# Performance work log

Measured on AMD Instinct MI355X. Metric: run time of the kernel, lower is better.

The kernel has to match this reference:

```python
import jax, jax.numpy as jnp
from jax import lax
import numpy as np

ROI = 7  # roi_size


def _extract_rois(feat, coords):
    """Faithful port of extract_roi_features: clamp a 7x7 window to image bounds,
    then bilinearly resize the (possibly smaller) crop back to 7x7
    (F.interpolate, mode='bilinear', align_corners=False)."""
    B, C, H, W = feat.shape
    half = ROI // 2

    def axis_idx(c, size):
        start = jnp.maximum(0, c - half)                  # [B,A]
        end = jnp.minimum(size, c + half + 1)
        Li = end - start                                  # crop length (int) [B,A]
        L = Li.astype(feat.dtype)[..., None]              # [B,A,1]
        j = jnp.arange(ROI, dtype=feat.dtype)
        # align_corners=False source coordinate, clamped into the crop
        src = jnp.clip((j + 0.5) * L / ROI - 0.5, 0.0, L - 1.0)  # [B,A,7]
        i0 = jnp.floor(src).astype(jnp.int32)
        i1 = jnp.minimum(i0 + 1, Li[..., None] - 1)
        w1 = src - i0.astype(feat.dtype)
        return start[..., None] + i0, start[..., None] + i1, 1.0 - w1, w1

    xc = coords[..., 0].astype(jnp.int32)
    yc = coords[..., 1].astype(jnp.int32)
    y0, y1, wy0, wy1 = axis_idx(yc, H)
    x0, x1, wx0, wx1 = axis_idx(xc, W)
    Bn, A = xc.shape
    bi = jnp.arange(Bn)[:, None, None, None]

    def g(Y, X):  # gather -> [B,A,7,7,C]
        return feat[bi, :, Y[:, :, :, None], X[:, :, None, :]]

    wy0 = wy0[:, :, :, None, None]; wy1 = wy1[:, :, :, None, None]
    wx0 = wx0[:, :, None, :, None]; wx1 = wx1[:, :, None, :, None]
    v = (wy0 * wx0 * g(y0, x0) + wy0 * wx1 * g(y0, x1)
         + wy1 * wx0 * g(y1, x0) + wy1 * wx1 * g(y1, x1))
    return jnp.transpose(v, (0, 1, 4, 2, 3))  # [B,A,C,7,7]


def _conv(x, w, b, pad):
    y = lax.conv_general_dilated(x, w, (1, 1), [(pad, pad), (pad, pad)],
                                 dimension_numbers=('NCHW', 'OIHW', 'NCHW'))
    return y + b[None, :, None, None]


def _bn(x, scale, bias, mean, var, eps=1e-5):
    inv = scale * lax.rsqrt(var + eps)
    return x * inv[None, :, None, None] + (bias - mean * inv)[None, :, None, None]


def setup_inputs() -> dict:
    key = jax.random.key(0)
    ks = jax.random.split(key, 12)
    B, A, C, H, W = 8, 128, 256, 64, 64
    f32 = jnp.float32
    d = {}
    d['feat_rgb'] = jax.random.normal(ks[0], (B, C, H, W), f32)
    d['feat_tir'] = jax.random.normal(ks[1], (B, C, H, W), f32)
    d['anchor_coords'] = jax.random.randint(ks[2], (B, A, 2), 0, 64).astype(jnp.int32)
    # local_fusion: Conv(2C->C,3) BN ReLU Conv(C->C,3) BN ReLU
    d['conv1_w'] = jax.random.normal(ks[3], (C, 2 * C, 3, 3), f32) * 0.02
    d['conv1_b'] = jnp.zeros((C,), f32)
    d['bn1_scale'] = jnp.ones((C,), f32)
    d['bn1_bias'] = jnp.zeros((C,), f32)
    d['bn1_mean'] = jax.random.normal(ks[4], (C,), f32) * 0.1
    d['bn1_var'] = jax.random.uniform(ks[5], (C,), f32, 0.5, 1.5)
    d['conv2_w'] = jax.random.normal(ks[6], (C, C, 3, 3), f32) * 0.02
    d['conv2_b'] = jnp.zeros((C,), f32)
    d['bn2_scale'] = jnp.ones((C,), f32)
    d['bn2_bias'] = jnp.zeros((C,), f32)
    d['bn2_mean'] = jax.random.normal(ks[7], (C,), f32) * 0.1
    d['bn2_var'] = jax.random.uniform(ks[8], (C,), f32, 0.5, 1.5)
    # weight_generator: Conv(C->C//4,1) ReLU Conv(C//4->2,1) Softmax(dim=1)
    d['wg1_w'] = jax.random.normal(ks[9], (C // 4, C, 1, 1), f32) * 0.05
    d['wg1_b'] = jnp.zeros((C // 4,), f32)
    d['wg2_w'] = jax.random.normal(ks[10], (2, C // 4, 1, 1), f32) * 0.05
    d['wg2_b'] = jnp.zeros((2,), f32)
    return d


def reference(feat_rgb, feat_tir, anchor_coords,
              conv1_w, conv1_b, bn1_scale, bn1_bias, bn1_mean, bn1_var,
              conv2_w, conv2_b, bn2_scale, bn2_bias, bn2_mean, bn2_var,
              wg1_w, wg1_b, wg2_w, wg2_b):
    B, C, H, W = feat_rgb.shape
    A = anchor_coords.shape[1]
    roi_rgb = _extract_rois(feat_rgb, anchor_coords)  # [B,A,C,7,7]
    roi_tir = _extract_rois(feat_tir, anchor_coords)
    rgb = roi_rgb.reshape(B * A, C, ROI, ROI)
    tir = roi_tir.reshape(B * A, C, ROI, ROI)
    x = jnp.concatenate([rgb, tir], axis=1)           # [B*A, 2C, 7, 7]
    x = jax.nn.relu(_bn(_conv(x, conv1_w, conv1_b, 1), bn1_scale, bn1_bias, bn1_mean, bn1_var))
    x = jax.nn.relu(_bn(_conv(x, conv2_w, conv2_b, 1), bn2_scale, bn2_bias, bn2_mean, bn2_var))
    h = jax.nn.relu(_conv(x, wg1_w, wg1_b, 0))
    w = jax.nn.softmax(_conv(h, wg2_w, wg2_b, 0), axis=1)  # [B*A, 2, 7, 7]
    fused = w[:, 0:1] * rgb + w[:, 1:2] * tir
    return fused.reshape(B, A, C, ROI, ROI)
```

## Files before the change

### kernel.cpp

```cpp
#include <hip/hip_runtime.h>
#include <cstddef>
#include <cstdint>


typedef unsigned int u32;
typedef unsigned short u16;
typedef __attribute__((ext_vector_type(8))) short short8;
typedef __attribute__((ext_vector_type(4))) float float4v;

__device__ __forceinline__ float bf2f(u16 u) {
  u32 x = ((u32)u) << 16;
  return __builtin_bit_cast(float, x);
}
__device__ __forceinline__ u16 f2bf(float f) {
  u32 x = __builtin_bit_cast(u32, f);
  x = x + 0x7fffu + ((x >> 16) & 1u);
  return (u16)(x >> 16);
}
__device__ __forceinline__ void gl_lds16(const void* g, void* l) {
  __builtin_amdgcn_global_load_lds((const __attribute__((address_space(1))) void*)g,
                                   (__attribute__((address_space(3))) void*)l, 16, 0, 0);
}

template <int IC>
__global__ void k_prep_w(const float* __restrict__ w, u16* __restrict__ wt) {
  int i = blockIdx.x * 256 + threadIdx.x;
  if (i >= 9 * 256 * IC) return;
  int t = i / (256 * IC);
  int rem = i - t * 256 * IC;
  int oc = rem / IC, ic = rem - oc * IC;
  wt[i] = f2bf(w[((size_t)oc * IC + ic) * 9 + t]);
}

__global__ void k_prep_bn(const float* __restrict__ cb, const float* __restrict__ sc,
                          const float* __restrict__ bi, const float* __restrict__ mn,
                          const float* __restrict__ vr, float* __restrict__ sb) {
  int c = threadIdx.x;
  float inv = sc[c] * rsqrtf(vr[c] + 1e-5f);
  sb[c]       = inv;
  sb[256 + c] = cb[c] * inv + (bi[c] - mn[c] * inv);
}

__global__ __launch_bounds__(256)
void k_roi2(const float* __restrict__ frgb, const float* __restrict__ ftir,
            const int* __restrict__ coords, u16* __restrict__ cat) {
  int ba = blockIdx.x, b = ba >> 7, tid = threadIdx.x;
  __shared__ int   si0[2][7], si1[2][7];
  __shared__ float sw0[2][7], sw1[2][7];
  __shared__ u16 tile[49][514];
  if (tid < 14) {
    int axis = tid / 7;
    int j = tid - axis * 7;
    int c = coords[ba * 2 + (axis == 0 ? 1 : 0)];
    int start = max(0, c - 3);
    int end   = min(64, c + 4);
    int Li = end - start;
    float L = (float)Li;
    float src = ((float)j + 0.5f) * L / 7.0f - 0.5f;
    src = fminf(fmaxf(src, 0.0f), L - 1.0f);
    int i0 = (int)floorf(src);
    int i1 = min(i0 + 1, Li - 1);
    float w1 = src - (float)i0;
    si0[axis][j] = start + i0;
    si1[axis][j] = start + i1;
    sw0[axis][j] = 1.0f - w1;
    sw1[axis][j] = w1;
  }
  __syncthreads();
  const float* fr = frgb + (size_t)b * 256 * 4096;
  const float* ft = ftir + (size_t)b * 256 * 4096;
  for (int idx = tid; idx < 256 * 49; idx += 256) {
    int c = idx / 49, p = idx - c * 49;
    int jy = p / 7, jx = p - (p / 7) * 7;
    int y0 = si0[0][jy], y1 = si1[0][jy];
    int x0 = si1[1][jx], x1b = si1[1][jx];
    x0 = si0[1][jx]; x1b = si1[1][jx];
    float wy0 = sw0[0][jy], wy1 = sw1[0][jy];
    float wx0 = sw0[1][jx], wx1 = sw1[1][jx];
    float a00 = wy0 * wx0, a01 = wy0 * wx1, a10 = wy1 * wx0, a11 = wy1 * wx1;
    const float* fc = fr + (size_t)c * 4096;
    float vr_ = a00 * fc[y0 * 64 + x0] + a01 * fc[y0 * 64 + x1b] +
                a10 * fc[y1 * 64 + x0] + a11 * fc[y1 * 64 + x1b];
    const float* gc = ft + (size_t)c * 4096;
    float vt_ = a00 * gc[y0 * 64 + x0] + a01 * gc[y0 * 64 + x1b] +
                a10 * gc[y1 * 64 + x0] + a11 * gc[y1 * 64 + x1b];
    tile[p][c]       = f2bf(vr_);
    tile[p][256 + c] = f2bf(vt_);
  }
  __syncthreads();
  u16* dst = cat + (size_t)ba * 81 * 512;
  for (int o = tid; o < 81 * 512; o += 256) {
    int row = o >> 9, c = o & 511;
    int py0 = row / 9, px0 = row - (row / 9) * 9;
    u16 v = 0;
    if (py0 >= 1 && py0 <= 7 && px0 >= 1 && px0 <= 7)
      v = tile[(py0 - 1) * 7 + (px0 - 1)][c];
    dst[o] = v;
  }
}

template <int ICT, bool FIRST>
__global__ __launch_bounds__(256)
void k_conv_mfma(const u16* __restrict__ IN, const u16* __restrict__ WT,
                 const float* __restrict__ sb, u16* __restrict__ OUT) {
  constexpr int NC = ICT / 64;
  constexpr int CHB = 81 * 128;
  __shared__ u16 lds[2][CHB / 2];
  const int tid = threadIdx.x;
  const int lane = tid & 63, wv = tid >> 6;
  const int l15 = lane & 15, hi = lane >> 4;
  const int ba = blockIdx.x;
  const u16* src = IN + (size_t)ba * 81 * ICT;

  if (FIRST) {
    u16* ob = OUT + (size_t)ba * 81 * 256;
#pragma unroll
    for (int i = 0; i < 32; ++i) {
      int row = (i < 9) ? i : (i < 18) ? (63 + i)
                                       : (9 * ((i - 18) / 2 + 1) + ((i - 18) & 1) * 8);
      ob[row * 256 + tid] = 0;
    }
  }

  int py[4], px[4], pvalid[4];
#pragma unroll
  for (int pf = 0; pf < 4; ++pf) {
    int pix = pf * 16 + l15;
    pvalid[pf] = (pix < 49) ? 1 : 0;
    py[pf] = pix / 7;
    px[pf] = pix - (pix / 7) * 7;
  }

  float4v acc[4][4];
#pragma unroll
  for (int a = 0; a < 4; ++a)
#pragma unroll
    for (int b = 0; b < 4; ++b) acc[a][b] = (float4v){0.f, 0.f, 0.f, 0.f};

  auto stage = [&](int ch, int buf) {
    const char* cbase = (const char*)(src + ch * 64);
    for (int s = wv; s < 11; s += 4) {
      int o = (s * 64 + lane) * 16;
      if (o < CHB) {
        int u = o ^ (((o >> 7) & 7) << 4);
        int row = u >> 7, cb = u & 127;
        gl_lds16(cbase + (size_t)row * (ICT * 2) + cb,
                 (char*)&lds[buf][0] + s * 1024);
      }
    }
  };

  stage(0, 0);
  __syncthreads();

  const int woc = wv * 64;
#pragma unroll 1
  for (int ch = 0; ch < NC; ++ch) {
    const int cur = ch & 1;
    if (ch + 1 < NC) stage(ch + 1, cur ^ 1);
    const u16* lb = &lds[cur][0];
#pragma unroll
    for (int t = 0; t < 9; ++t) {
      const int dy = t / 3, dx = t - (t / 3) * 3;
      int r[4];
#pragma unroll
      for (int pf = 0; pf < 4; ++pf)
        r[pf] = pvalid[pf] ? ((py[pf] + dy) * 9 + px[pf] + dx) : 0;
#pragma unroll
      for (int kk = 0; kk < 2; ++kk) {
        short8 bfr[4], wfr[4];
#pragma unroll
        for (int pf = 0; pf < 4; ++pf) {
          int ub = r[pf] * 128 + kk * 64 + hi * 16;
          int sw = ub ^ ((r[pf] & 7) << 4);
          bfr[pf] = *(const short8*)((const char*)lb + sw);
        }
#pragma unroll
        for (int f = 0; f < 4; ++f) {
          size_t wofs = ((size_t)(t * 256 + woc + f * 16 + l15)) * ICT +
                        ch * 64 + kk * 32 + hi * 8;
          wfr[f] = *(const short8*)(WT + wofs);
        }
#pragma unroll
        for (int pf = 0; pf < 4; ++pf)
#pragma unroll
          for (int f = 0; f < 4; ++f)
            acc[pf][f] = FIRST
                ? __builtin_amdgcn_mfma_f32_16x16x32_bf16(bfr[pf], wfr[f], acc[pf][f], 0, 0, 0)
                : __builtin_amdgcn_mfma_f32_16x16x32_bf16(wfr[f], bfr[pf], acc[pf][f], 0, 0, 0);
      }
    }
    __syncthreads();
  }

  if (FIRST) {
    u16* ob = OUT + (size_t)ba * 81 * 256;
#pragma unroll
    for (int f = 0; f < 4; ++f) {
      int oc = woc + f * 16 + l15;
      float s = sb[oc], bb = sb[256 + oc];
#pragma unroll
      for (int pf = 0; pf < 4; ++pf)
#pragma unroll
        for (int reg = 0; reg < 4; ++reg) {
          int pix = pf * 16 + hi * 4 + reg;
          if (pix < 49) {
            int pp = (pix / 7 + 1) * 9 + (pix - (pix / 7) * 7) + 1;
            ob[pp * 256 + oc] = f2bf(fmaxf(acc[pf][f][reg] * s + bb, 0.0f));
          }
        }
    }
  } else {
    u16* ob = OUT + (size_t)ba * 256 * 49;
#pragma unroll
    for (int f = 0; f < 4; ++f)
#pragma unroll
      for (int reg = 0; reg < 4; ++reg) {
        int oc = woc + f * 16 + hi * 4 + reg;
        float s = sb[oc], bb = sb[256 + oc];
#pragma unroll
        for (int pf = 0; pf < 4; ++pf) {
          int pix = pf * 16 + l15;
          if (pix < 49)
            ob[(size_t)oc * 49 + pix] = f2bf(fmaxf(acc[pf][f][reg] * s + bb, 0.0f));
        }
      }
  }
}

__global__ __launch_bounds__(256)
void k_head_fuse(const u16* __restrict__ x3, const u16* __restrict__ cat,
                 const float* __restrict__ w1, const float* __restrict__ b1,
                 const float* __restrict__ w2, const float* __restrict__ b2,
                 float* __restrict__ out) {
  int ba  = blockIdx.x;
  int tid = threadIdx.x;
  __shared__ float xs[256 * 49];
  __shared__ float hs[64 * 49];
  __shared__ float ls[2 * 49];
  __shared__ float swx[2 * 49];
  const u16* src = x3 + (size_t)ba * 256 * 49;
  for (int idx = tid; idx < 256 * 49; idx += 256) xs[idx] = bf2f(src[idx]);
  __syncthreads();
  for (int idx = tid; idx < 64 * 49; idx += 256) {
    int oh = idx / 49, p = idx - oh * 49;
    float s = b1[oh];
    const float* wr = w1 + oh * 256;
    for (int ic = 0; ic < 256; ++ic) s += wr[ic] * xs[ic * 49 + p];
    hs[idx] = fmaxf(s, 0.0f);
  }
  __syncthreads();
  if (tid < 98) {
    int chn = tid / 49, p = tid - chn * 49;
    float s = b2[chn];
    const float* wr = w2 + chn * 64;
    for (int k = 0; k < 64; ++k) s += wr[k] * hs[k * 49 + p];
    ls[tid] = s;
  }
  __syncthreads();
  if (tid < 49) {
    float l0 = ls[tid], l1 = ls[49 + tid];
    float m = fmaxf(l0, l1);
    float e0 = expf(l0 - m), e1 = expf(l1 - m);
    float d = e0 + e1;
    swx[tid]      = e0 / d;
    swx[49 + tid] = e1 / d;
  }
  __syncthreads();
  const u16* cr = cat + (size_t)ba * 81 * 512;
  float* o = out + (size_t)ba * 256 * 49;
  for (int idx = tid; idx < 256 * 49; idx += 256) {
    int c = idx / 49, p = idx - (idx / 49) * 49;
    int pp = (p / 7 + 1) * 9 + (p - (p / 7) * 7) + 1;
    float rgb = bf2f(cr[pp * 512 + c]);
    float tir = bf2f(cr[pp * 512 + 256 + c]);
    o[idx] = swx[p] * rgb + swx[49 + p] * tir;
  }
}

extern "C" void kernel_launch(void* const* d_in, const int* in_sizes, int n_in,
                              void* d_out, int out_size, void* d_ws, size_t ws_size,
                              hipStream_t stream) {
  const float* feat_rgb = (const float*)d_in[0];
  const float* feat_tir = (const float*)d_in[1];
  const int*   coords   = (const int*)d_in[2];
  const float* conv1_w  = (const float*)d_in[3];
  const float* conv1_b  = (const float*)d_in[4];
  const float* bn1_s    = (const float*)d_in[5];
  const float* bn1_b    = (const float*)d_in[6];
  const float* bn1_m    = (const float*)d_in[7];
  const float* bn1_v    = (const float*)d_in[8];
  const float* conv2_w  = (const float*)d_in[9];
  const float* conv2_b  = (const float*)d_in[10];
  const float* bn2_s    = (const float*)d_in[11];
  const float* bn2_b    = (const float*)d_in[12];
  const float* bn2_m    = (const float*)d_in[13];
  const float* bn2_v    = (const float*)d_in[14];
  const float* wg1_w    = (const float*)d_in[15];
  const float* wg1_b    = (const float*)d_in[16];
  const float* wg2_w    = (const float*)d_in[17];
  const float* wg2_b    = (const float*)d_in[18];
  float* out = (float*)d_out;

  char* base = (char*)d_ws;
  u16*   W1T  = (u16*)(base);
  u16*   W2T  = (u16*)(base + 2359296);
  float* SB1  = (float*)(base + 2359296 + 1179648);
  float* SB2  = (float*)(base + 2359296 + 1179648 + 2048);
  u16*   CAT2 = (u16*)(base + 2359296 + 1179648 + 4096);
  u16*   X2   = (u16*)(base + 2359296 + 1179648 + 4096 + 84934656);
  u16*   X3   = (u16*)(base + 2359296 + 1179648 + 4096 + 84934656 + 42467328);

  k_prep_w<512><<<(9 * 256 * 512 + 255) / 256, 256, 0, stream>>>(conv1_w, W1T);
  k_prep_w<256><<<(9 * 256 * 256 + 255) / 256, 256, 0, stream>>>(conv2_w, W2T);
  k_prep_bn<<<1, 256, 0, stream>>>(conv1_b, bn1_s, bn1_b, bn1_m, bn1_v, SB1);
  k_prep_bn<<<1, 256, 0, stream>>>(conv2_b, bn2_s, bn2_b, bn2_m, bn2_v, SB2);
  k_roi2<<<1024, 256, 0, stream>>>(feat_rgb, feat_tir, coords, CAT2);
  k_conv_mfma<512, true><<<1024, 256, 0, stream>>>(CAT2, W1T, SB1, X2);
  k_conv_mfma<256, false><<<1024, 256, 0, stream>>>(X2, W2T, SB2, X3);
  k_head_fuse<<<1024, 256, 0, stream>>>(X3, CAT2, wg1_w, wg1_b, wg2_w, wg2_b, out);
}
```

Baseline: 739.3 us.

## Process two ROIs per conv block with 8 waves and prefetched weight fragments

The conv MFMA kernel now handles two ROIs per block with 512 threads. Each wave covers 32 output channels across 98 pixels (7 pixel fragments × 2 channel fragments) instead of 64 channels × 49 pixels, so each weight fragment load is reused across more pixels and less weight traffic goes to global/L2. Weight fragments are double-buffered one step ahead, and MFMA groups are wrapped in s_setprio. The cost is a larger LDS footprint (two ROIs per buffer) and more accumulator registers, which may limit occupancy. The ROI kernel also gets a small cleanup of a redundant index assignment.

```diff
diff --git a/kernel.cpp b/kernel.cpp
--- a/kernel.cpp
+++ b/kernel.cpp
@@ -73,17 +73,16 @@
     int c = idx / 49, p = idx - c * 49;
     int jy = p / 7, jx = p - (p / 7) * 7;
     int y0 = si0[0][jy], y1 = si1[0][jy];
-    int x0 = si1[1][jx], x1b = si1[1][jx];
-    x0 = si0[1][jx]; x1b = si1[1][jx];
+    int x0 = si0[1][jx], x1 = si1[1][jx];
     float wy0 = sw0[0][jy], wy1 = sw1[0][jy];
     float wx0 = sw0[1][jx], wx1 = sw1[1][jx];
     float a00 = wy0 * wx0, a01 = wy0 * wx1, a10 = wy1 * wx0, a11 = wy1 * wx1;
     const float* fc = fr + (size_t)c * 4096;
-    float vr_ = a00 * fc[y0 * 64 + x0] + a01 * fc[y0 * 64 + x1b] +
-                a10 * fc[y1 * 64 + x0] + a11 * fc[y1 * 64 + x1b];
+    float vr_ = a00 * fc[y0 * 64 + x0] + a01 * fc[y0 * 64 + x1] +
+                a10 * fc[y1 * 64 + x0] + a11 * fc[y1 * 64 + x1];
     const float* gc = ft + (size_t)c * 4096;
-    float vt_ = a00 * gc[y0 * 64 + x0] + a01 * gc[y0 * 64 + x1b] +
-                a10 * gc[y1 * 64 + x0] + a11 * gc[y1 * 64 + x1b];
+    float vt_ = a00 * gc[y0 * 64 + x0] + a01 * gc[y0 * 64 + x1] +
+                a10 * gc[y1 * 64 + x0] + a11 * gc[y1 * 64 + x1];
     tile[p][c]       = f2bf(vr_);
     tile[p][256 + c] = f2bf(vt_);
   }
@@ -100,52 +99,57 @@
 }
 
 template <int ICT, bool FIRST>
-__global__ __launch_bounds__(256)
+__global__ __launch_bounds__(512, 4)
 void k_conv_mfma(const u16* __restrict__ IN, const u16* __restrict__ WT,
                  const float* __restrict__ sb, u16* __restrict__ OUT) {
   constexpr int NC = ICT / 64;
-  constexpr int CHB = 81 * 128;
-  __shared__ u16 lds[2][CHB / 2];
+  constexpr int BUFB = 2 * 81 * 128;
+  __shared__ __align__(16) u16 lds[2][BUFB / 2];
   const int tid = threadIdx.x;
   const int lane = tid & 63, wv = tid >> 6;
   const int l15 = lane & 15, hi = lane >> 4;
-  const int ba = blockIdx.x;
-  const u16* src = IN + (size_t)ba * 81 * ICT;
+  const int ba2 = blockIdx.x * 2;
+  const char* inb = (const char*)IN;
 
   if (FIRST) {
-    u16* ob = OUT + (size_t)ba * 81 * 256;
+    int oc = tid & 255, rh = tid >> 8;
+    u16* ob = OUT + ((size_t)(ba2 + rh) * 81) * 256 + oc;
 #pragma unroll
     for (int i = 0; i < 32; ++i) {
       int row = (i < 9) ? i : (i < 18) ? (63 + i)
                                        : (9 * ((i - 18) / 2 + 1) + ((i - 18) & 1) * 8);
-      ob[row * 256 + tid] = 0;
+      ob[row * 256] = 0;
     }
   }
 
-  int py[4], px[4], pvalid[4];
-#pragma unroll
-  for (int pf = 0; pf < 4; ++pf) {
-    int pix = pf * 16 + l15;
-    pvalid[pf] = (pix < 49) ? 1 : 0;
-    py[pf] = pix / 7;
-    px[pf] = pix - (pix / 7) * 7;
-  }
-
-  float4v acc[4][4];
-#pragma unroll
-  for (int a = 0; a < 4; ++a)
-#pragma unroll
-    for (int b = 0; b < 4; ++b) acc[a][b] = (float4v){0.f, 0.f, 0.f, 0.f};
+  int rg[7];
+#pragma unroll
+  for (int pf = 0; pf < 7; ++pf) {
+    int P = pf * 16 + l15;
+    if (P > 97) P = 97;
+    int roi = (P >= 49) ? 1 : 0;
+    int q = P - roi * 49;
+    rg[pf] = roi * 81 + (q / 7) * 9 + (q - (q / 7) * 7);
+  }
+
+  float4v acc[7][2];
+#pragma unroll
+  for (int a = 0; a < 7; ++a)
+#pragma unroll
+    for (int f = 0; f < 2; ++f) acc[a][f] = (float4v){0.f, 0.f, 0.f, 0.f};
 
   auto stage = [&](int ch, int buf) {
-    const char* cbase = (const char*)(src + ch * 64);
-    for (int s = wv; s < 11; s += 4) {
-      int o = (s * 64 + lane) * 16;
-      if (o < CHB) {
-        int u = o ^ (((o >> 7) & 7) << 4);
-        int row = u >> 7, cb = u & 127;
-        gl_lds16(cbase + (size_t)row * (ICT * 2) + cb,
-                 (char*)&lds[buf][0] + s * 1024);
+    for (int s = wv; s < 21; s += 8) {
+      int d = s * 1024 + lane * 16;
+      if (d < BUFB) {
+        int u = d ^ (((d >> 7) & 7) << 4);
+        int row_g = u >> 7;
+        int col = u & 127;
+        int roi = (row_g >= 81) ? 1 : 0;
+        int rr = row_g - roi * 81;
+        const char* src = inb + ((size_t)(ba2 + roi) * 81 + rr) * (ICT * 2) +
+                          ch * 128 + col;
+        gl_lds16(src, (char*)&lds[buf][0] + s * 1024);
       }
     }
   };
@@ -153,76 +157,89 @@
   stage(0, 0);
   __syncthreads();
 
-  const int woc = wv * 64;
+  const int wlane = (wv * 32 + l15) * ICT + hi * 8;
+
+  int cur = 0;
 #pragma unroll 1
   for (int ch = 0; ch < NC; ++ch) {
-    const int cur = ch & 1;
     if (ch + 1 < NC) stage(ch + 1, cur ^ 1);
-    const u16* lb = &lds[cur][0];
-#pragma unroll
-    for (int t = 0; t < 9; ++t) {
+    const char* lb = (const char*)&lds[cur][0];
+    const u16* wch = WT + wlane + ch * 64;
+    short8 wfr[2][2];
+#pragma unroll
+    for (int f = 0; f < 2; ++f)
+      wfr[0][f] = *(const short8*)(wch + (f * 16) * ICT);
+#pragma unroll
+    for (int j = 0; j < 18; ++j) {
+      const int t = j >> 1, kk = j & 1;
       const int dy = t / 3, dx = t - (t / 3) * 3;
-      int r[4];
-#pragma unroll
-      for (int pf = 0; pf < 4; ++pf)
-        r[pf] = pvalid[pf] ? ((py[pf] + dy) * 9 + px[pf] + dx) : 0;
-#pragma unroll
-      for (int kk = 0; kk < 2; ++kk) {
-        short8 bfr[4], wfr[4];
-#pragma unroll
-        for (int pf = 0; pf < 4; ++pf) {
-          int ub = r[pf] * 128 + kk * 64 + hi * 16;
-          int sw = ub ^ ((r[pf] & 7) << 4);
-          bfr[pf] = *(const short8*)((const char*)lb + sw);
-        }
-#pragma unroll
-        for (int f = 0; f < 4; ++f) {
-          size_t wofs = ((size_t)(t * 256 + woc + f * 16 + l15)) * ICT +
-                        ch * 64 + kk * 32 + hi * 8;
-          wfr[f] = *(const short8*)(WT + wofs);
-        }
-#pragma unroll
-        for (int pf = 0; pf < 4; ++pf)
-#pragma unroll
-          for (int f = 0; f < 4; ++f)
-            acc[pf][f] = FIRST
-                ? __builtin_amdgcn_mfma_f32_16x16x32_bf16(bfr[pf], wfr[f], acc[pf][f], 0, 0, 0)
-                : __builtin_amdgcn_mfma_f32_16x16x32_bf16(wfr[f], bfr[pf], acc[pf][f], 0, 0, 0);
+      if (j < 17) {
+        const int t2 = (j + 1) >> 1, k2 = (j + 1) & 1;
+#pragma unroll
+        for (int f = 0; f < 2; ++f)
+          wfr[(j + 1) & 1][f] =
+              *(const short8*)(wch + (t2 * 256 + f * 16) * ICT + k2 * 32);
       }
+      short8 bfr[7];
+#pragma unroll
+      for (int pf = 0; pf < 7; ++pf) {
+        int rr = rg[pf] + dy * 9 + dx;
+        int byt = (rr * 128 + kk * 64 + hi * 16) ^ ((rr & 7) << 4);
+        bfr[pf] = *(const short8*)(lb + byt);
+      }
+      __builtin_amdgcn_s_setprio(1);
+#pragma unroll
+      for (int pf = 0; pf < 7; ++pf)
+#pragma unroll
+        for (int f = 0; f < 2; ++f)
+          acc[pf][f] = FIRST
+              ? __builtin_amdgcn_mfma_f32_16x16x32_bf16(bfr[pf], wfr[j & 1][f],
+                                                        acc[pf][f], 0, 0, 0)
+              : __builtin_amdgcn_mfma_f32_16x16x32_bf16(wfr[j & 1][f], bfr[pf],
+                                                        acc[pf][f], 0, 0, 0);
+      __builtin_amdgcn_s_setprio(0);
     }
     __syncthreads();
+    cur ^= 1;
   }
 
   if (FIRST) {
-    u16* ob = OUT + (size_t)ba * 81 * 256;
-#pragma unroll
-    for (int f = 0; f < 4; ++f) {
-      int oc = woc + f * 16 + l15;
+    u16* ob = OUT + (size_t)ba2 * 81 * 256;
+#pragma unroll
+    for (int f = 0; f < 2; ++f) {
+      int oc = wv * 32 + f * 16 + l15;
       float s = sb[oc], bb = sb[256 + oc];
 #pragma unroll
-      for (int pf = 0; pf < 4; ++pf)
+      for (int pf = 0; pf < 7; ++pf)
 #pragma unroll
         for (int reg = 0; reg < 4; ++reg) {
-          int pix = pf * 16 + hi * 4 + reg;
-          if (pix < 49) {
-            int pp = (pix / 7 + 1) * 9 + (pix - (pix / 7) * 7) + 1;
-            ob[pp * 256 + oc] = f2bf(fmaxf(acc[pf][f][reg] * s + bb, 0.0f));
+          int P = pf * 16 + hi * 4 + reg;
+          if (P < 98) {
+            int roi = (P >= 49) ? 1 : 0;
+            int q = P - roi * 49;
+            int pp = (q / 7 + 1) * 9 + (q - (q / 7) * 7) + 1;
+            ob[((size_t)roi * 81 + pp) * 256 + oc] =
+                f2bf(fmaxf(acc[pf][f][reg] * s + bb, 0.0f));
           }
         }
     }
   } else {
-    u16* ob = OUT + (size_t)ba * 256 * 49;
-#pragma unroll
-    for (int f = 0; f < 4; ++f)
+    u16* ob = OUT + (size_t)ba2 * 256 * 49;
+#pragma unroll
+    for (int f = 0; f < 2; ++f)
 #pragma unroll
       for (int reg = 0; reg < 4; ++reg) {
-        int oc = woc + f * 16 + hi * 4 + reg;
+        int oc = wv * 32 + f * 16 + hi * 4 + reg;
         float s = sb[oc], bb = sb[256 + oc];
 #pragma unroll
-        for (int pf = 0; pf < 4; ++pf) {
-          int pix = pf * 16 + l15;
-          if (pix < 49)
-            ob[(size_t)oc * 49 + pix] = f2bf(fmaxf(acc[pf][f][reg] * s + bb, 0.0f));
+        for (int pf = 0; pf < 7; ++pf) {
+          int P = pf * 16 + l15;
+          if (P < 98) {
+            int roi = (P >= 49) ? 1 : 0;
+            int q = P - roi * 49;
+            ob[((size_t)roi * 256 + oc) * 49 + q] =
+                f2bf(fmaxf(acc[pf][f][reg] * s + bb, 0.0f));
+          }
         }
       }
   }
@@ -316,7 +333,7 @@
   k_prep_bn<<<1, 256, 0, stream>>>(conv1_b, bn1_s, bn1_b, bn1_m, bn1_v, SB1);
   k_prep_bn<<<1, 256, 0, stream>>>(conv2_b, bn2_s, bn2_b, bn2_m, bn2_v, SB2);
   k_roi2<<<1024, 256, 0, stream>>>(feat_rgb, feat_tir, coords, CAT2);
-  k_conv_mfma<512, true><<<1024, 256, 0, stream>>>(CAT2, W1T, SB1, X2);
-  k_conv_mfma<256, false><<<1024, 256, 0, stream>>>(X2, W2T, SB2, X3);
+  k_conv_mfma<512, true><<<512, 512, 0, stream>>>(CAT2, W1T, SB1, X2);
+  k_conv_mfma<256, false><<<512, 512, 0, stream>>>(X2, W2T, SB2, X3);
   k_head_fuse<<<1024, 256, 0, stream>>>(X3, CAT2, wg1_w, wg1_b, wg2_w, wg2_b, out);
 }
```

After: 746.6 us. Within noise of the previous version (+1.0%).
